# Performance work log

Hardware: AMD Instinct MI355X
Metric: run time of the kernel (lower is better)

Reference implementation:

```python
import jax, jax.numpy as jnp
import numpy as np

NUM_HEADS = 16
LORA_SCALE = 16.0 / 8.0  # alpha / rank


def setup_inputs() -> dict:
    key = jax.random.key(0)
    ks = jax.random.split(key, 9)
    B, N, C, R = 8, 1024, 1024, 8
    return {
        "x": jax.random.normal(ks[0], (B, N, C), dtype=jnp.float32),
        "qkv_w": jax.random.normal(ks[1], (3 * C, C), dtype=jnp.float32) * (C ** -0.5),
        "qkv_b": jax.random.normal(ks[2], (3 * C,), dtype=jnp.float32) * 0.02,
        "proj_w": jax.random.normal(ks[3], (C, C), dtype=jnp.float32) * (C ** -0.5),
        "proj_b": jax.random.normal(ks[4], (C,), dtype=jnp.float32) * 0.02,
        "lora_q_a": jax.random.normal(ks[5], (R, C), dtype=jnp.float32) * (C ** -0.5),
        "lora_q_b": jnp.zeros((C, R), dtype=jnp.float32) + jax.random.normal(ks[6], (C, R), dtype=jnp.float32) * 0.01,
        "lora_v_a": jax.random.normal(ks[7], (R, C), dtype=jnp.float32) * (C ** -0.5),
        "lora_v_b": jax.random.normal(ks[8], (C, R), dtype=jnp.float32) * 0.01,
    }


def reference(x, qkv_w, qkv_b, proj_w, proj_b, lora_q_a, lora_q_b, lora_v_a, lora_v_b):
    B, N, C = x.shape
    H = NUM_HEADS
    D = C // H
    scale = D ** -0.5

    # fused QKV projection: [B,N,3C] -> [3,B,H,N,D]
    qkv = (x @ qkv_w.T + qkv_b).reshape(B, N, 3, H, D).transpose(2, 0, 3, 1, 4)
    q, k, v = qkv[0], qkv[1], qkv[2]

    # LoRA adapters on q and v (dropout=0 in eval): x @ A^T @ B^T * (alpha/rank)
    q_adapt = ((x @ lora_q_a.T) @ lora_q_b.T) * LORA_SCALE
    q = q + q_adapt.reshape(B, N, H, D).transpose(0, 2, 1, 3)
    v_adapt = ((x @ lora_v_a.T) @ lora_v_b.T) * LORA_SCALE
    v = v + v_adapt.reshape(B, N, H, D).transpose(0, 2, 1, 3)

    # manual softmax attention
    attn = jax.nn.softmax(jnp.einsum("bhnd,bhmd->bhnm", q, k) * scale, axis=-1)
    out = jnp.einsum("bhnm,bhmd->bhnd", attn, v)  # [B,H,N,D]
    out = out.transpose(0, 2, 1, 3).reshape(B, N, C)
    return out @ proj_w.T + proj_b
```

## Files before the change

kernel.cpp:

```cpp
#include <hip/hip_runtime.h>

typedef unsigned short u16;
typedef __bf16 bf16x8 __attribute__((ext_vector_type(8)));
typedef float f32x4 __attribute__((ext_vector_type(4)));
typedef u16 u16x4 __attribute__((ext_vector_type(4)));
typedef u16 u16x8 __attribute__((ext_vector_type(8)));

#define MFMA_B16(a, b, c) __builtin_amdgcn_mfma_f32_16x16x32_bf16((a), (b), (c), 0, 0, 0)

__device__ __forceinline__ u16 f2b(float f) {
  unsigned int b = __builtin_bit_cast(unsigned int, f);
  b += 0x7FFFu + ((b >> 16) & 1u);
  return (u16)(b >> 16);
}

__device__ __forceinline__ void gload16(const void* g, void* l) {
  __builtin_amdgcn_global_load_lds(
      (const __attribute__((address_space(1))) unsigned int*)g,
      (__attribute__((address_space(3))) unsigned int*)l, 16, 0, 0);
}

__device__ __forceinline__ int swzK(int row, int col) {
  return row * 64 + (col ^ ((row & 7) << 3));
}
__device__ __forceinline__ int swzP(int row, int col) {
  return row * 128 + (col ^ ((row & 7) << 3));
}
__device__ __forceinline__ int swzV(int d, int kv) {
  return d * 128 + (kv ^ ((((d >> 3) ^ d) & 7) << 3));
}

__global__ void k_cast(const float* __restrict__ s, u16* __restrict__ d, int n) {
  int i = blockIdx.x * blockDim.x + threadIdx.x;
  const int stride = gridDim.x * blockDim.x;
  const int n4 = n >> 2;
  for (; i < n4; i += stride) {
    f32x4 v = *(const f32x4*)(s + (size_t)i * 4);
    u16x4 o = {f2b(v[0]), f2b(v[1]), f2b(v[2]), f2b(v[3])};
    *(u16x4*)(d + (size_t)i * 4) = o;
  }
}

__global__ void k_prep_x(const float* __restrict__ x, const float* __restrict__ qa,
                         const float* __restrict__ va, u16* __restrict__ xb,
                         float* __restrict__ tq, float* __restrict__ tv) {
  const int gw = (blockIdx.x * blockDim.x + threadIdx.x) >> 6;
  const int lane = threadIdx.x & 63;
  const float* xr = x + (size_t)gw * 1024;
  u16* xo = xb + (size_t)gw * 1024;
  float acc[16];
#pragma unroll
  for (int r = 0; r < 16; ++r) acc[r] = 0.f;
#pragma unroll
  for (int p = 0; p < 4; ++p) {
    const int c = p * 256 + lane * 4;
    f32x4 v = *(const f32x4*)(xr + c);
    u16x4 o = {f2b(v[0]), f2b(v[1]), f2b(v[2]), f2b(v[3])};
    *(u16x4*)(xo + c) = o;
#pragma unroll
    for (int r = 0; r < 8; ++r) {
      const float* qr = qa + r * 1024 + c;
      const float* vr = va + r * 1024 + c;
      acc[r]     += v[0] * qr[0] + v[1] * qr[1] + v[2] * qr[2] + v[3] * qr[3];
      acc[r + 8] += v[0] * vr[0] + v[1] * vr[1] + v[2] * vr[2] + v[3] * vr[3];
    }
  }
#pragma unroll
  for (int r = 0; r < 16; ++r) {
#pragma unroll
    for (int off = 1; off < 64; off <<= 1) acc[r] += __shfl_xor(acc[r], off, 64);
  }
  if (lane < 8) tq[gw * 8 + lane] = acc[lane];
  else if (lane < 16) tv[gw * 8 + (lane - 8)] = acc[lane];
}

__global__ __launch_bounds__(256, 2)
void k_qkv(const u16* __restrict__ A, const u16* __restrict__ Bw,
           const float* __restrict__ bias,
           const float* __restrict__ tq, const float* __restrict__ tv,
           const float* __restrict__ lqb, const float* __restrict__ lvb,
           u16* __restrict__ Qo, u16* __restrict__ Ko, u16* __restrict__ Vo) {
  __shared__ alignas(16) u16 lA[128 * 64];
  __shared__ alignas(16) u16 lB[128 * 64];
  const int t = threadIdx.x;
  const int w = t >> 6, lane = t & 63;
  const int wr = w >> 1, wc = w & 1;
  const int bm = blockIdx.x & 63, bn = blockIdx.x >> 6;
  const int rowg = bm * 128, colg = bn * 128;
  const int srow = t >> 3, scol = (t & 7) * 8;

  f32x4 acc[4][4];
#pragma unroll
  for (int i = 0; i < 4; ++i)
#pragma unroll
    for (int j = 0; j < 4; ++j) acc[i][j] = 0.0f;

  for (int kt = 0; kt < 16; ++kt) {
#pragma unroll
    for (int c = 0; c < 4; ++c) {
      const int row = c * 32 + srow;
      gload16(A + (size_t)(rowg + row) * 1024 + kt * 64 + scol, &lA[row * 64 + scol]);
      gload16(Bw + (size_t)(colg + row) * 1024 + kt * 64 + scol, &lB[row * 64 + scol]);
    }
    __syncthreads();
#pragma unroll
    for (int kk = 0; kk < 2; ++kk) {
      bf16x8 af[4], bfr[4];
#pragma unroll
      for (int i = 0; i < 4; ++i) {
        af[i]  = *(const bf16x8*)&lA[(wr * 64 + i * 16 + (lane & 15)) * 64 + kk * 32 + (lane >> 4) * 8];
        bfr[i] = *(const bf16x8*)&lB[(wc * 64 + i * 16 + (lane & 15)) * 64 + kk * 32 + (lane >> 4) * 8];
      }
#pragma unroll
      for (int i = 0; i < 4; ++i)
#pragma unroll
        for (int j = 0; j < 4; ++j) acc[i][j] = MFMA_B16(af[i], bfr[j], acc[i][j]);
    }
    __syncthreads();
  }

  const int sec = bn >> 3;
  float* lT = (float*)lA;
  float* lLB = (float*)lB;
  const float* tvec = (sec == 2) ? tv : tq;
  const float* lb = (sec == 2) ? lvb : lqb;
  if (t < 128) {
    const float* s = tvec + (size_t)(rowg + t) * 8;
    *(f32x4*)&lT[t * 8] = *(const f32x4*)s;
    *(f32x4*)&lT[t * 8 + 4] = *(const f32x4*)(s + 4);
  } else {
    const int cc = t - 128;
    const float* s = lb + (size_t)((colg & 1023) + cc) * 8;
    *(f32x4*)&lLB[cc * 8] = *(const f32x4*)s;
    *(f32x4*)&lLB[cc * 8 + 4] = *(const f32x4*)(s + 4);
  }
  __syncthreads();

  const float SQ = 0.18033688011112042f;
  float bvl[4], lbc[4][8];
  int cll[4];
#pragma unroll
  for (int j = 0; j < 4; ++j) {
    cll[j] = wc * 64 + j * 16 + (lane & 15);
    bvl[j] = bias[colg + cll[j]];
#pragma unroll
    for (int r = 0; r < 8; ++r) lbc[j][r] = lLB[cll[j] * 8 + r];
  }
  u16* outp = (sec == 0) ? Qo : ((sec == 1) ? Ko : Vo);
#pragma unroll
  for (int i = 0; i < 4; ++i) {
#pragma unroll
    for (int rg = 0; rg < 4; ++rg) {
      const int rl = wr * 64 + i * 16 + (lane >> 4) * 4 + rg;
      const int grow = rowg + rl;
      const int bb = grow >> 10, nidx = grow & 1023;
      float tr[8];
      if (sec != 1) {
#pragma unroll
        for (int r = 0; r < 8; ++r) tr[r] = lT[rl * 8 + r];
      }
#pragma unroll
      for (int j = 0; j < 4; ++j) {
        float v = acc[i][j][rg] + bvl[j];
        if (sec != 1) {
          float ad = 0.f;
#pragma unroll
          for (int r = 0; r < 8; ++r) ad += tr[r] * lbc[j][r];
          v += 2.0f * ad;
        }
        if (sec == 0) v *= SQ;
        const int c1024 = (colg & 1023) + cll[j];
        const int h = c1024 >> 6, d = c1024 & 63;
        outp[(size_t)((bb * 16 + h) * 1024 + nidx) * 64 + d] = f2b(v);
      }
    }
  }
}

__global__ __launch_bounds__(256, 2)
void k_attn(const u16* __restrict__ Qb, const u16* __restrict__ Kb,
            const u16* __restrict__ Vb, u16* __restrict__ att) {
  __shared__ alignas(16) u16 lsP[128 * 128];
  __shared__ alignas(16) u16 lsK[128 * 64];
  __shared__ alignas(16) u16 lsVT[64 * 128];
  const int t = threadIdx.x, w = t >> 6, lane = t & 63;
  const int bh = blockIdx.x >> 3, qt = blockIdx.x & 7;
  const u16* Qg = Qb + (size_t)bh * 65536;
  const u16* Kg = Kb + (size_t)bh * 65536;
  const u16* Vg = Vb + (size_t)bh * 65536;
  const int srow = t >> 3, scol = (t & 7) * 8;
  const int srcc = (((t & 7) ^ (t >> 3)) & 7) * 8;

#pragma unroll
  for (int c = 0; c < 4; ++c) {
    const int row = c * 32 + srow;
    gload16(Qg + (size_t)(qt * 128 + row) * 64 + srcc, &lsP[row * 64 + scol]);
  }
  __syncthreads();
  bf16x8 qf[2][2];
#pragma unroll
  for (int mf = 0; mf < 2; ++mf)
#pragma unroll
    for (int kk = 0; kk < 2; ++kk)
      qf[mf][kk] = *(const bf16x8*)&lsP[swzK(w * 32 + mf * 16 + (lane & 15),
                                             kk * 32 + (lane >> 4) * 8)];

  float mi[2][4], li[2][4];
  f32x4 oacc[2][4];
#pragma unroll
  for (int mf = 0; mf < 2; ++mf) {
#pragma unroll
    for (int rg = 0; rg < 4; ++rg) { mi[mf][rg] = -1e30f; li[mf][rg] = 0.f; }
#pragma unroll
    for (int df = 0; df < 4; ++df) oacc[mf][df] = 0.0f;
  }

  for (int kt = 0; kt < 8; ++kt) {
#pragma unroll
    for (int c = 0; c < 4; ++c) {
      const int row = c * 32 + srow;
      gload16(Kg + (size_t)(kt * 128 + row) * 64 + srcc, &lsK[row * 64 + scol]);
    }
#pragma unroll
    for (int p = 0; p < 4; ++p) {
      const int kv = p * 32 + srow;
      u16x8 vv = *(const u16x8*)(Vg + (size_t)(kt * 128 + kv) * 64 + scol);
#pragma unroll
      for (int i = 0; i < 8; ++i) lsVT[swzV(scol + i, kv)] = vv[i];
    }
    __syncthreads();

    f32x4 sacc[2][8];
#pragma unroll
    for (int mf = 0; mf < 2; ++mf)
#pragma unroll
      for (int nf = 0; nf < 8; ++nf) sacc[mf][nf] = 0.0f;
#pragma unroll
    for (int kk = 0; kk < 2; ++kk) {
#pragma unroll
      for (int nf = 0; nf < 8; ++nf) {
        bf16x8 kf = *(const bf16x8*)&lsK[swzK(nf * 16 + (lane & 15),
                                              kk * 32 + (lane >> 4) * 8)];
#pragma unroll
        for (int mf = 0; mf < 2; ++mf) sacc[mf][nf] = MFMA_B16(qf[mf][kk], kf, sacc[mf][nf]);
      }
    }

#pragma unroll
    for (int mf = 0; mf < 2; ++mf) {
#pragma unroll
      for (int rg = 0; rg < 4; ++rg) {
        float mx = sacc[mf][0][rg];
#pragma unroll
        for (int nf = 1; nf < 8; ++nf) mx = fmaxf(mx, sacc[mf][nf][rg]);
#pragma unroll
        for (int off = 1; off < 16; off <<= 1) mx = fmaxf(mx, __shfl_xor(mx, off, 64));
        const float mnew = fmaxf(mi[mf][rg], mx);
        const float alpha = exp2f(mi[mf][rg] - mnew);
        float rs = 0.f;
#pragma unroll
        for (int nf = 0; nf < 8; ++nf) {
          const float p = exp2f(sacc[mf][nf][rg] - mnew);
          sacc[mf][nf][rg] = p;
          rs += p;
        }
#pragma unroll
        for (int off = 1; off < 16; off <<= 1) rs += __shfl_xor(rs, off, 64);
        li[mf][rg] = li[mf][rg] * alpha + rs;
        mi[mf][rg] = mnew;
#pragma unroll
        for (int df = 0; df < 4; ++df) oacc[mf][df][rg] *= alpha;
      }
    }

#pragma unroll
    for (int mf = 0; mf < 2; ++mf)
#pragma unroll
      for (int nf = 0; nf < 8; ++nf)
#pragma unroll
        for (int rg = 0; rg < 4; ++rg)
          lsP[swzP(w * 32 + mf * 16 + (lane >> 4) * 4 + rg, nf * 16 + (lane & 15))] =
              f2b(sacc[mf][nf][rg]);

    asm volatile("s_waitcnt lgkmcnt(0)" ::: "memory");

    bf16x8 pa[2][4];
#pragma unroll
    for (int mf = 0; mf < 2; ++mf)
#pragma unroll
      for (int kk = 0; kk < 4; ++kk)
        pa[mf][kk] = *(const bf16x8*)&lsP[swzP(w * 32 + mf * 16 + (lane & 15),
                                               kk * 32 + (lane >> 4) * 8)];
#pragma unroll
    for (int df = 0; df < 4; ++df) {
#pragma unroll
      for (int kk = 0; kk < 4; ++kk) {
        bf16x8 vf = *(const bf16x8*)&lsVT[swzV(df * 16 + (lane & 15),
                                               kk * 32 + (lane >> 4) * 8)];
#pragma unroll
        for (int mf = 0; mf < 2; ++mf) oacc[mf][df] = MFMA_B16(pa[mf][kk], vf, oacc[mf][df]);
      }
    }
    __syncthreads();
  }

  const int bb = bh >> 4, h = bh & 15;
#pragma unroll
  for (int mf = 0; mf < 2; ++mf) {
#pragma unroll
    for (int rg = 0; rg < 4; ++rg) {
      const float rl = 1.0f / li[mf][rg];
      const int qrow = qt * 128 + w * 32 + mf * 16 + (lane >> 4) * 4 + rg;
      const size_t base = ((size_t)(bb * 1024 + qrow)) * 1024 + h * 64;
#pragma unroll
      for (int df = 0; df < 4; ++df)
        att[base + df * 16 + (lane & 15)] = f2b(oacc[mf][df][rg] * rl);
    }
  }
}

__global__ __launch_bounds__(256, 2)
void k_proj(const u16* __restrict__ A, const u16* __restrict__ Bw,
            const float* __restrict__ bias, float* __restrict__ out) {
  __shared__ alignas(16) u16 lA[128 * 64];
  __shared__ alignas(16) u16 lB[128 * 64];
  const int t = threadIdx.x;
  const int w = t >> 6, lane = t & 63;
  const int wr = w >> 1, wc = w & 1;
  const int bm = blockIdx.x & 63, bn = blockIdx.x >> 6;
  const int rowg = bm * 128, colg = bn * 128;
  const int srow = t >> 3, scol = (t & 7) * 8;

  f32x4 acc[4][4];
#pragma unroll
  for (int i = 0; i < 4; ++i)
#pragma unroll
    for (int j = 0; j < 4; ++j) acc[i][j] = 0.0f;

  for (int kt = 0; kt < 16; ++kt) {
#pragma unroll
    for (int c = 0; c < 4; ++c) {
      const int row = c * 32 + srow;
      gload16(A + (size_t)(rowg + row) * 1024 + kt * 64 + scol, &lA[row * 64 + scol]);
      gload16(Bw + (size_t)(colg + row) * 1024 + kt * 64 + scol, &lB[row * 64 + scol]);
    }
    __syncthreads();
#pragma unroll
    for (int kk = 0; kk < 2; ++kk) {
      bf16x8 af[4], bfr[4];
#pragma unroll
      for (int i = 0; i < 4; ++i) {
        af[i]  = *(const bf16x8*)&lA[(wr * 64 + i * 16 + (lane & 15)) * 64 + kk * 32 + (lane >> 4) * 8];
        bfr[i] = *(const bf16x8*)&lB[(wc * 64 + i * 16 + (lane & 15)) * 64 + kk * 32 + (lane >> 4) * 8];
      }
#pragma unroll
      for (int i = 0; i < 4; ++i)
#pragma unroll
        for (int j = 0; j < 4; ++j) acc[i][j] = MFMA_B16(af[i], bfr[j], acc[i][j]);
    }
    __syncthreads();
  }

#pragma unroll
  for (int i = 0; i < 4; ++i) {
#pragma unroll
    for (int rg = 0; rg < 4; ++rg) {
      const int grow = rowg + wr * 64 + i * 16 + (lane >> 4) * 4 + rg;
#pragma unroll
      for (int j = 0; j < 4; ++j) {
        const int cl = wc * 64 + j * 16 + (lane & 15);
        out[(size_t)grow * 1024 + colg + cl] = acc[i][j][rg] + bias[colg + cl];
      }
    }
  }
}

extern "C" void kernel_launch(void* const* d_in, const int* in_sizes, int n_in,
                              void* d_out, int out_size, void* d_ws, size_t ws_size,
                              hipStream_t stream) {
  (void)in_sizes; (void)n_in; (void)out_size; (void)ws_size;
  const float* x      = (const float*)d_in[0];
  const float* qkv_w  = (const float*)d_in[1];
  const float* qkv_b  = (const float*)d_in[2];
  const float* proj_w = (const float*)d_in[3];
  const float* proj_b = (const float*)d_in[4];
  const float* lqa    = (const float*)d_in[5];
  const float* lqb    = (const float*)d_in[6];
  const float* lva    = (const float*)d_in[7];
  const float* lvb    = (const float*)d_in[8];
  float* out = (float*)d_out;
  char* ws = (char*)d_ws;

  u16* xb    = (u16*)(ws);
  u16* wqkv  = (u16*)(ws + (size_t)(16u << 20));
  u16* wproj = (u16*)(ws + (size_t)(22u << 20));
  float* tq  = (float*)(ws + (size_t)(24u << 20));
  float* tv  = (float*)(ws + (size_t)(24u << 20) + (256u << 10));
  u16* Qb    = (u16*)(ws + (size_t)(25u << 20));
  u16* Kb    = (u16*)(ws + (size_t)(41u << 20));
  u16* Vb    = (u16*)(ws + (size_t)(57u << 20));
  u16* att   = (u16*)(ws + (size_t)(73u << 20));

  k_cast<<<dim3(1024), dim3(256), 0, stream>>>(qkv_w, wqkv, 3072 * 1024);
  k_cast<<<dim3(512), dim3(256), 0, stream>>>(proj_w, wproj, 1024 * 1024);
  k_prep_x<<<dim3(2048), dim3(256), 0, stream>>>(x, lqa, lva, xb, tq, tv);
  k_qkv<<<dim3(1536), dim3(256), 0, stream>>>(xb, wqkv, qkv_b, tq, tv, lqb, lvb, Qb, Kb, Vb);
  k_attn<<<dim3(1024), dim3(256), 0, stream>>>(Qb, Kb, Vb, att);
  k_proj<<<dim3(512), dim3(256), 0, stream>>>(att, wproj, proj_b, out);
}
```

Measured before the change: 387.7 us.

## Keep attention probabilities in registers via transposed QK^T and lazy rescaling

The attention kernel now computes S^T (K as the A operand) so each lane holds a full query column. Probabilities can then be packed to bf16 with v_cvt_pk_bf16_f32 and fed straight into the PV MFMA, which removes the LDS round trip for P. V^T is stored with a permuted kv index to match this register layout. The online softmax rescale is skipped unless the running max grows by more than 8 (in log2 units), and the freed LDS allows three blocks per CU instead of two. The trade-offs are extra shuffles to redistribute alpha and l, and a bounded risk of overflow in the deferred-max scheme.

```diff
diff --git a/kernel.cpp b/kernel.cpp
--- a/kernel.cpp
+++ b/kernel.cpp
@@ -5,6 +5,7 @@
 typedef float f32x4 __attribute__((ext_vector_type(4)));
 typedef u16 u16x4 __attribute__((ext_vector_type(4)));
 typedef u16 u16x8 __attribute__((ext_vector_type(8)));
+typedef unsigned int u32x4 __attribute__((ext_vector_type(4)));
 
 #define MFMA_B16(a, b, c) __builtin_amdgcn_mfma_f32_16x16x32_bf16((a), (b), (c), 0, 0, 0)
 
@@ -14,6 +15,12 @@
   return (u16)(b >> 16);
 }
 
+__device__ __forceinline__ unsigned int cvtpk(float lo, float hi) {
+  unsigned int r;
+  asm("v_cvt_pk_bf16_f32 %0, %1, %2" : "=v"(r) : "v"(lo), "v"(hi));
+  return r;
+}
+
 __device__ __forceinline__ void gload16(const void* g, void* l) {
   __builtin_amdgcn_global_load_lds(
       (const __attribute__((address_space(1))) unsigned int*)g,
@@ -23,11 +30,8 @@
 __device__ __forceinline__ int swzK(int row, int col) {
   return row * 64 + (col ^ ((row & 7) << 3));
 }
-__device__ __forceinline__ int swzP(int row, int col) {
-  return row * 128 + (col ^ ((row & 7) << 3));
-}
-__device__ __forceinline__ int swzV(int d, int kv) {
-  return d * 128 + (kv ^ ((((d >> 3) ^ d) & 7) << 3));
+__device__ __forceinline__ int swzVT(int d, int s) {
+  return d * 128 + (s ^ ((((d >> 3) ^ d) & 7) << 3));
 }
 
 __global__ void k_cast(const float* __restrict__ s, u16* __restrict__ d, int n) {
@@ -177,10 +181,9 @@
   }
 }
 
-__global__ __launch_bounds__(256, 2)
+__global__ __launch_bounds__(256, 3)
 void k_attn(const u16* __restrict__ Qb, const u16* __restrict__ Kb,
             const u16* __restrict__ Vb, u16* __restrict__ att) {
-  __shared__ alignas(16) u16 lsP[128 * 128];
   __shared__ alignas(16) u16 lsK[128 * 64];
   __shared__ alignas(16) u16 lsVT[64 * 128];
   const int t = threadIdx.x, w = t >> 6, lane = t & 63;
@@ -190,11 +193,12 @@
   const u16* Vg = Vb + (size_t)bh * 65536;
   const int srow = t >> 3, scol = (t & 7) * 8;
   const int srcc = (((t & 7) ^ (t >> 3)) & 7) * 8;
+  const int g = lane >> 4, q16 = lane & 15;
 
 #pragma unroll
   for (int c = 0; c < 4; ++c) {
     const int row = c * 32 + srow;
-    gload16(Qg + (size_t)(qt * 128 + row) * 64 + srcc, &lsP[row * 64 + scol]);
+    gload16(Qg + (size_t)(qt * 128 + row) * 64 + srcc, &lsK[row * 64 + scol]);
   }
   __syncthreads();
   bf16x8 qf[2][2];
@@ -202,15 +206,15 @@
   for (int mf = 0; mf < 2; ++mf)
 #pragma unroll
     for (int kk = 0; kk < 2; ++kk)
-      qf[mf][kk] = *(const bf16x8*)&lsP[swzK(w * 32 + mf * 16 + (lane & 15),
-                                             kk * 32 + (lane >> 4) * 8)];
-
-  float mi[2][4], li[2][4];
+      qf[mf][kk] = *(const bf16x8*)&lsK[swzK(w * 32 + mf * 16 + q16, kk * 32 + g * 8)];
+  __syncthreads();
+
+  float mi[2], li[2];
   f32x4 oacc[2][4];
 #pragma unroll
   for (int mf = 0; mf < 2; ++mf) {
-#pragma unroll
-    for (int rg = 0; rg < 4; ++rg) { mi[mf][rg] = -1e30f; li[mf][rg] = 0.f; }
+    mi[mf] = -1e30f;
+    li[mf] = 0.f;
 #pragma unroll
     for (int df = 0; df < 4; ++df) oacc[mf][df] = 0.0f;
   }
@@ -225,8 +229,9 @@
     for (int p = 0; p < 4; ++p) {
       const int kv = p * 32 + srow;
       u16x8 vv = *(const u16x8*)(Vg + (size_t)(kt * 128 + kv) * 64 + scol);
-#pragma unroll
-      for (int i = 0; i < 8; ++i) lsVT[swzV(scol + i, kv)] = vv[i];
+      const int s = ((kv >> 5) << 5) | ((((kv >> 2) & 3)) << 3) | ((((kv >> 4) & 1)) << 2) | (kv & 3);
+#pragma unroll
+      for (int i = 0; i < 8; ++i) lsVT[swzVT(scol + i, s)] = vv[i];
     }
     __syncthreads();
 
@@ -239,66 +244,76 @@
     for (int kk = 0; kk < 2; ++kk) {
 #pragma unroll
       for (int nf = 0; nf < 8; ++nf) {
-        bf16x8 kf = *(const bf16x8*)&lsK[swzK(nf * 16 + (lane & 15),
-                                              kk * 32 + (lane >> 4) * 8)];
-#pragma unroll
-        for (int mf = 0; mf < 2; ++mf) sacc[mf][nf] = MFMA_B16(qf[mf][kk], kf, sacc[mf][nf]);
-      }
-    }
-
+        bf16x8 kf = *(const bf16x8*)&lsK[swzK(nf * 16 + q16, kk * 32 + g * 8)];
+#pragma unroll
+        for (int mf = 0; mf < 2; ++mf) sacc[mf][nf] = MFMA_B16(kf, qf[mf][kk], sacc[mf][nf]);
+      }
+    }
+
+    float pmax[2];
 #pragma unroll
     for (int mf = 0; mf < 2; ++mf) {
-#pragma unroll
-      for (int rg = 0; rg < 4; ++rg) {
-        float mx = sacc[mf][0][rg];
-#pragma unroll
-        for (int nf = 1; nf < 8; ++nf) mx = fmaxf(mx, sacc[mf][nf][rg]);
-#pragma unroll
-        for (int off = 1; off < 16; off <<= 1) mx = fmaxf(mx, __shfl_xor(mx, off, 64));
-        const float mnew = fmaxf(mi[mf][rg], mx);
-        const float alpha = exp2f(mi[mf][rg] - mnew);
-        float rs = 0.f;
-#pragma unroll
-        for (int nf = 0; nf < 8; ++nf) {
-          const float p = exp2f(sacc[mf][nf][rg] - mnew);
-          sacc[mf][nf][rg] = p;
-          rs += p;
+      float mx = sacc[mf][0][0];
+#pragma unroll
+      for (int nf = 0; nf < 8; ++nf)
+#pragma unroll
+        for (int rg = 0; rg < 4; ++rg) mx = fmaxf(mx, sacc[mf][nf][rg]);
+      mx = fmaxf(mx, __shfl_xor(mx, 16, 64));
+      mx = fmaxf(mx, __shfl_xor(mx, 32, 64));
+      pmax[mf] = mx;
+    }
+    const int need = (pmax[0] - mi[0] > 8.f) || (pmax[1] - mi[1] > 8.f);
+    if (__any(need)) {
+#pragma unroll
+      for (int mf = 0; mf < 2; ++mf) {
+        const float mnew = fmaxf(mi[mf], pmax[mf]);
+        const float alpha = exp2f(mi[mf] - mnew);
+        li[mf] *= alpha;
+        mi[mf] = mnew;
+        float ar[4];
+#pragma unroll
+        for (int rg = 0; rg < 4; ++rg) ar[rg] = __shfl(alpha, (lane & 48) | (g * 4 + rg), 64);
+#pragma unroll
+        for (int df = 0; df < 4; ++df)
+#pragma unroll
+          for (int rg = 0; rg < 4; ++rg) oacc[mf][df][rg] *= ar[rg];
+      }
+    }
+#pragma unroll
+    for (int mf = 0; mf < 2; ++mf) {
+      float rs = 0.f;
+#pragma unroll
+      for (int nf = 0; nf < 8; ++nf)
+#pragma unroll
+        for (int rg = 0; rg < 4; ++rg) {
+          const float pv = exp2f(sacc[mf][nf][rg] - mi[mf]);
+          sacc[mf][nf][rg] = pv;
+          rs += pv;
         }
-#pragma unroll
-        for (int off = 1; off < 16; off <<= 1) rs += __shfl_xor(rs, off, 64);
-        li[mf][rg] = li[mf][rg] * alpha + rs;
-        mi[mf][rg] = mnew;
-#pragma unroll
-        for (int df = 0; df < 4; ++df) oacc[mf][df][rg] *= alpha;
-      }
-    }
-
-#pragma unroll
-    for (int mf = 0; mf < 2; ++mf)
-#pragma unroll
-      for (int nf = 0; nf < 8; ++nf)
-#pragma unroll
-        for (int rg = 0; rg < 4; ++rg)
-          lsP[swzP(w * 32 + mf * 16 + (lane >> 4) * 4 + rg, nf * 16 + (lane & 15))] =
-              f2b(sacc[mf][nf][rg]);
-
-    asm volatile("s_waitcnt lgkmcnt(0)" ::: "memory");
-
-    bf16x8 pa[2][4];
-#pragma unroll
-    for (int mf = 0; mf < 2; ++mf)
-#pragma unroll
-      for (int kk = 0; kk < 4; ++kk)
-        pa[mf][kk] = *(const bf16x8*)&lsP[swzP(w * 32 + mf * 16 + (lane & 15),
-                                               kk * 32 + (lane >> 4) * 8)];
-#pragma unroll
-    for (int df = 0; df < 4; ++df) {
-#pragma unroll
-      for (int kk = 0; kk < 4; ++kk) {
-        bf16x8 vf = *(const bf16x8*)&lsVT[swzV(df * 16 + (lane & 15),
-                                               kk * 32 + (lane >> 4) * 8)];
-#pragma unroll
-        for (int mf = 0; mf < 2; ++mf) oacc[mf][df] = MFMA_B16(pa[mf][kk], vf, oacc[mf][df]);
+      rs += __shfl_xor(rs, 16, 64);
+      rs += __shfl_xor(rs, 32, 64);
+      li[mf] += rs;
+    }
+
+#pragma unroll
+    for (int kk = 0; kk < 4; ++kk) {
+      bf16x8 pa[2];
+#pragma unroll
+      for (int mf = 0; mf < 2; ++mf) {
+        u32x4 pw;
+        pw[0] = cvtpk(sacc[mf][2 * kk][0], sacc[mf][2 * kk][1]);
+        pw[1] = cvtpk(sacc[mf][2 * kk][2], sacc[mf][2 * kk][3]);
+        pw[2] = cvtpk(sacc[mf][2 * kk + 1][0], sacc[mf][2 * kk + 1][1]);
+        pw[3] = cvtpk(sacc[mf][2 * kk + 1][2], sacc[mf][2 * kk + 1][3]);
+        pa[mf] = __builtin_bit_cast(bf16x8, pw);
+      }
+#pragma unroll
+      for (int df = 0; df < 4; ++df) {
+        const int dd = df * 16 + q16;
+        const int vkey = ((dd >> 3) ^ dd) & 7;
+        bf16x8 vfr = *(const bf16x8*)&lsVT[dd * 128 + ((kk * 32 + g * 8) ^ (vkey << 3))];
+#pragma unroll
+        for (int mf = 0; mf < 2; ++mf) oacc[mf][df] = MFMA_B16(pa[mf], vfr, oacc[mf][df]);
       }
     }
     __syncthreads();
@@ -307,14 +322,17 @@
   const int bb = bh >> 4, h = bh & 15;
 #pragma unroll
   for (int mf = 0; mf < 2; ++mf) {
+    float lr[4];
+#pragma unroll
+    for (int rg = 0; rg < 4; ++rg) lr[rg] = __shfl(li[mf], (lane & 48) | (g * 4 + rg), 64);
 #pragma unroll
     for (int rg = 0; rg < 4; ++rg) {
-      const float rl = 1.0f / li[mf][rg];
-      const int qrow = qt * 128 + w * 32 + mf * 16 + (lane >> 4) * 4 + rg;
+      const float rl = 1.0f / lr[rg];
+      const int qrow = qt * 128 + w * 32 + mf * 16 + g * 4 + rg;
       const size_t base = ((size_t)(bb * 1024 + qrow)) * 1024 + h * 64;
 #pragma unroll
       for (int df = 0; df < 4; ++df)
-        att[base + df * 16 + (lane & 15)] = f2b(oacc[mf][df][rg] * rl);
+        att[base + df * 16 + q16] = f2b(oacc[mf][df][rg] * rl);
     }
   }
 }
```

Measured after the change: 428.5 us. 10.5% more time.
